# Kernel tuning notes

Measured on AMD Instinct MI355X. Metric: run time of the kernel, lower is better.

## Reference

```python
import jax, jax.numpy as jnp
import numpy as np

H = 16
D = 64  # head_dim = 1024 // 16
SCALE = D ** -0.5


def setup_inputs() -> dict:
    key = jax.random.key(0)
    ks = jax.random.split(key, 12)
    B, N, C = 2, 2048, 1024
    s = C ** -0.5
    return {
        "hidden_states": jax.random.normal(ks[0], (B, N, C), jnp.float32),
        "pos_embeds": jax.random.normal(ks[1], (B, N, C), jnp.float32),
        "Wq": jax.random.normal(ks[2], (C, C), jnp.float32) * s,
        "bq": jnp.zeros((C,), jnp.float32),
        "Wk": jax.random.normal(ks[3], (C, C), jnp.float32) * s,
        "bk": jnp.zeros((C,), jnp.float32),
        "Wv": jax.random.normal(ks[4], (C, C), jnp.float32) * s,
        "bv": jnp.zeros((C,), jnp.float32),
        "Wpos": jax.random.normal(ks[5], (C, C), jnp.float32) * s,
        "pos_bias_u": jax.random.normal(ks[6], (H, D), jnp.float32) * 0.1,
        "pos_bias_v": jax.random.normal(ks[7], (H, D), jnp.float32) * 0.1,
        "Wo": jax.random.normal(ks[8], (C, C), jnp.float32) * s,
        "bo": jnp.zeros((C,), jnp.float32),
    }


def reference(hidden_states, pos_embeds, Wq, bq, Wk, bk, Wv, bv, Wpos,
              pos_bias_u, pos_bias_v, Wo, bo):
    B, N, C = hidden_states.shape
    # projections (torch Linear: y = x @ W.T + b), split heads -> (B, N, H, D)
    q = (hidden_states @ Wq.T + bq).reshape(B, N, H, D)
    k = (hidden_states @ Wk.T + bk).reshape(B, N, H, D)
    v = (hidden_states @ Wv.T + bv).reshape(B, N, H, D)
    p = (pos_embeds @ Wpos.T).reshape(B, N, H, D)
    # relative-position biased logits: matrix_ac + matrix_bd
    q_u = q + pos_bias_u  # (B,N,H,D) + (H,D)
    q_v = q + pos_bias_v
    ac = jnp.einsum('bnhd,bmhd->bhnm', q_u, k)
    bd = jnp.einsum('bnhd,bmhd->bhnm', q_v, p)
    attn = jax.nn.softmax((ac + bd) * SCALE, axis=-1)  # (B,H,N,N)
    out = jnp.einsum('bhnm,bmhd->bnhd', attn, v).reshape(B, N, C)
    return out @ Wo.T + bo
```

## Files before the change

kernel.cpp:

```cpp
#include <hip/hip_runtime.h>
#include <hip/hip_bf16.h>


typedef short bf16x8 __attribute__((ext_vector_type(8)));
typedef float f32x4 __attribute__((ext_vector_type(4)));

#define BB 2
#define NN 2048
#define CC 1024
#define HH 16
#define DD 64
#define MM (BB * NN)
#define SC2E 0.18033688f

__device__ __forceinline__ unsigned short f2bf(float f) {
    union { float f; unsigned int u; } x; x.f = f;
    unsigned int r = x.u + 0x7FFFu + ((x.u >> 16) & 1u);
    return (unsigned short)(r >> 16);
}

__device__ __forceinline__ float bf2f(unsigned short s) {
    union { unsigned int u; float f; } x; x.u = ((unsigned int)s) << 16;
    return x.f;
}

__device__ __forceinline__ unsigned int pk2(float a, float b) {
    __hip_bfloat162 h = __float22bfloat162_rn(make_float2(a, b));
    unsigned int u; __builtin_memcpy(&u, &h, 4); return u;
}

typedef __attribute__((address_space(1))) const unsigned int* gas1_t;
typedef __attribute__((address_space(3))) unsigned int* las3_t;

__device__ __forceinline__ void gload_lds16(const unsigned short* g, unsigned short* l) {
    __builtin_amdgcn_global_load_lds((gas1_t)g, (las3_t)l, 16, 0, 0);
}

__global__ __launch_bounds__(256) void cast_f32_bf16(const float* __restrict__ src,
                                                     unsigned short* __restrict__ dst,
                                                     int n4) {
    int i = blockIdx.x * 256 + threadIdx.x;
    if (i >= n4) return;
    float4 v = ((const float4*)src)[i];
    union { unsigned short s[4]; uint2 u; } p;
    p.s[0] = f2bf(v.x); p.s[1] = f2bf(v.y); p.s[2] = f2bf(v.z); p.s[3] = f2bf(v.w);
    ((uint2*)dst)[i] = p.u;
}

template <int MODE>
__global__ __launch_bounds__(256) void gemm_bt(const unsigned short* __restrict__ A,
                                               const unsigned short* __restrict__ B,
                                               void* __restrict__ out0,
                                               const void* __restrict__ aux,
                                               const float* __restrict__ bias) {
    constexpr int K = CC;
    __shared__ unsigned short As[128 * 32];
    __shared__ unsigned short Bs[64 * 32];
    const int t = threadIdx.x;
    const int w = t >> 6, lane = t & 63, l15 = lane & 15, quad = lane >> 4;
    const int m0 = blockIdx.x * 128, n0 = blockIdx.y * 64;
    const int wm = (w >> 1) * 64, wn = (w & 1) * 32;

    f32x4 acc[4][2];
#pragma unroll
    for (int i = 0; i < 4; ++i)
#pragma unroll
        for (int j = 0; j < 2; ++j)
#pragma unroll
            for (int r = 0; r < 4; ++r) acc[i][j][r] = 0.f;

    for (int kb = 0; kb < K; kb += 32) {
        __syncthreads();
#pragma unroll
        for (int j = 0; j < 2; ++j) {
            int id = j * 256 + t;
            int row = id >> 2, c4 = id & 3;
            gload_lds16(&A[(size_t)(m0 + row) * K + kb + c4 * 8], &As[id * 8]);
        }
        {
            int row = t >> 2, c4 = t & 3;
            gload_lds16(&B[(size_t)(n0 + row) * K + kb + c4 * 8], &Bs[t * 8]);
        }
        __syncthreads();
        bf16x8 af[4], bfr[2];
#pragma unroll
        for (int i = 0; i < 4; ++i)
            af[i] = *(const bf16x8*)&As[(wm + i * 16 + l15) * 32 + quad * 8];
#pragma unroll
        for (int j = 0; j < 2; ++j)
            bfr[j] = *(const bf16x8*)&Bs[(wn + j * 16 + l15) * 32 + quad * 8];
#pragma unroll
        for (int i = 0; i < 4; ++i)
#pragma unroll
            for (int j = 0; j < 2; ++j)
                acc[i][j] = __builtin_amdgcn_mfma_f32_16x16x32_bf16(af[i], bfr[j], acc[i][j], 0, 0, 0);
    }

#pragma unroll
    for (int i = 0; i < 4; ++i) {
#pragma unroll
        for (int j = 0; j < 2; ++j) {
            const int col = n0 + wn + j * 16 + l15;
            const int row_base = m0 + wm + i * 16 + quad * 4;
            const float bc = (MODE == 4) ? 0.f : (bias ? bias[col] : 0.f);
            if (MODE == 0) {
#pragma unroll
                for (int r = 0; r < 4; ++r)
                    ((unsigned short*)out0)[(size_t)(row_base + r) * CC + col] = f2bf(acc[i][j][r] + bc);
            } else if (MODE == 1) {
#pragma unroll
                for (int r = 0; r < 4; ++r)
                    ((unsigned short*)out0)[(size_t)(row_base + r) * CC + col] =
                        f2bf((acc[i][j][r] + bc) * SC2E);
            } else if (MODE == 2) {
#pragma unroll
                for (int r = 0; r < 4; ++r)
                    ((float*)out0)[(size_t)(row_base + r) * CC + col] = acc[i][j][r] + bc;
            } else if (MODE == 4) {
#pragma unroll
                for (int r = 0; r < 4; ++r) {
                    float kv = bf2f(((const unsigned short*)aux)[(size_t)(row_base + r) * CC + col]);
                    ((unsigned short*)out0)[(size_t)(row_base + r) * CC + col] = f2bf(acc[i][j][r] + kv);
                }
            } else {
                const int b = row_base >> 11, nseq = row_base & 2047;
                const int hh = col >> 6, dd = col & 63;
                union { unsigned short s[4]; uint2 u; } pk;
#pragma unroll
                for (int r = 0; r < 4; ++r) pk.s[r] = f2bf(acc[i][j][r] + bc);
                size_t idx = ((size_t)(b * HH + hh) * DD + dd) * NN + nseq;
                *(uint2*)&((unsigned short*)out0)[idx] = pk.u;
            }
        }
    }
}

__global__ __launch_bounds__(256) void fuse_c(const unsigned short* __restrict__ k,
                                              const unsigned short* __restrict__ kp,
                                              const float* __restrict__ pbu,
                                              const float* __restrict__ pbv,
                                              float* __restrict__ c) {
    const int gw = (blockIdx.x * 256 + threadIdx.x) >> 6;
    const int lane = threadIdx.x & 63;
    const int row = gw >> 4, h = gw & 15;
    const size_t off = (size_t)row * CC + h * 64 + lane;
    const float u = pbu[h * 64 + lane], v = pbv[h * 64 + lane];
    float val = (u - v) * bf2f(k[off]) + v * bf2f(kp[off]);
#pragma unroll
    for (int o = 1; o < 64; o <<= 1) val += __shfl_xor(val, o);
    if (lane == 0) {
        const int b = row >> 11, n = row & 2047;
        c[((size_t)(b * HH + h)) * NN + n] = val * SC2E;
    }
}

#define PST 80
__global__ __launch_bounds__(256, 2) void attn_kernel(const unsigned short* __restrict__ q,
                                                      const unsigned short* __restrict__ kp,
                                                      const unsigned short* __restrict__ vt,
                                                      const float* __restrict__ cb,
                                                      unsigned short* __restrict__ att) {
    __shared__ unsigned short Ks[64 * 64];
    __shared__ unsigned short Vs[64 * 64];
    __shared__ unsigned short Ps[4][32 * PST];

    const int t = threadIdx.x;
    const int w = t >> 6, lane = t & 63, l15 = lane & 15, quad = lane >> 4;
    const int qt = blockIdx.x, h = blockIdx.y, b = blockIdx.z;
    const int sw = (l15 & 7) * 8;

    bf16x8 qf[2][2];
#pragma unroll
    for (int qb = 0; qb < 2; ++qb) {
        const int qrow = qt * 128 + w * 32 + qb * 16 + l15;
        const size_t qoff = ((size_t)(b * NN + qrow) * HH + h) * DD;
#pragma unroll
        for (int c2 = 0; c2 < 2; ++c2)
            qf[qb][c2] = *(const bf16x8*)&q[qoff + c2 * 32 + quad * 8];
    }

    f32x4 oT[4][2];
    float l_lane[2] = {0.f, 0.f};
#pragma unroll
    for (int db = 0; db < 4; ++db)
#pragma unroll
        for (int qb = 0; qb < 2; ++qb)
#pragma unroll
            for (int r = 0; r < 4; ++r) oT[db][qb][r] = 0.f;

    const size_t kbase = (size_t)b * NN * CC + (size_t)h * DD;
    const size_t vbase = (size_t)(b * HH + h) * DD * NN;
    const size_t cbase = (size_t)(b * HH + h) * NN;

    for (int kt = 0; kt < NN / 64; ++kt) {
        __syncthreads();
#pragma unroll
        for (int j = 0; j < 2; ++j) {
            int id = j * 256 + t, row = id >> 3, c8 = id & 7;
            int gc = (c8 ^ (row & 7)) * 8;
            gload_lds16(&kp[kbase + (size_t)(kt * 64 + row) * CC + gc], &Ks[id * 8]);
            gload_lds16(&vt[vbase + (size_t)row * NN + kt * 64 + gc], &Vs[id * 8]);
        }
        __syncthreads();

        f32x4 s[2][4];
#pragma unroll
        for (int t4 = 0; t4 < 4; ++t4) {
            f32x4 c4 = *(const f32x4*)&cb[cbase + kt * 64 + t4 * 16 + quad * 4];
            s[0][t4] = c4; s[1][t4] = c4;
        }
#pragma unroll
        for (int t4 = 0; t4 < 4; ++t4) {
            const int row = t4 * 16 + l15;
#pragma unroll
            for (int c2 = 0; c2 < 2; ++c2) {
                bf16x8 kf = *(const bf16x8*)&Ks[row * 64 + ((c2 * 4 + quad) * 8 ^ sw)];
#pragma unroll
                for (int qb = 0; qb < 2; ++qb)
                    s[qb][t4] = __builtin_amdgcn_mfma_f32_16x16x32_bf16(kf, qf[qb][c2], s[qb][t4], 0, 0, 0);
            }
        }

#pragma unroll
        for (int qb = 0; qb < 2; ++qb) {
            float rs = 0.f;
#pragma unroll
            for (int t4 = 0; t4 < 4; ++t4)
#pragma unroll
                for (int r = 0; r < 4; ++r) {
                    float pv = exp2f(s[qb][t4][r]);
                    s[qb][t4][r] = pv;
                    rs += pv;
                }
            l_lane[qb] += rs;
#pragma unroll
            for (int t4 = 0; t4 < 4; ++t4) {
                uint2 pk;
                pk.x = pk2(s[qb][t4][0], s[qb][t4][1]);
                pk.y = pk2(s[qb][t4][2], s[qb][t4][3]);
                *(uint2*)&Ps[w][(qb * 16 + l15) * PST + t4 * 16 + quad * 4] = pk;
            }
        }

#pragma unroll
        for (int c2 = 0; c2 < 2; ++c2) {
            bf16x8 pf[2];
#pragma unroll
            for (int qb = 0; qb < 2; ++qb)
                pf[qb] = *(const bf16x8*)&Ps[w][(qb * 16 + l15) * PST + c2 * 32 + quad * 8];
#pragma unroll
            for (int db = 0; db < 4; ++db) {
                bf16x8 vf = *(const bf16x8*)&Vs[(db * 16 + l15) * 64 + ((c2 * 4 + quad) * 8 ^ sw)];
#pragma unroll
                for (int qb = 0; qb < 2; ++qb)
                    oT[db][qb] = __builtin_amdgcn_mfma_f32_16x16x32_bf16(vf, pf[qb], oT[db][qb], 0, 0, 0);
            }
        }
    }

#pragma unroll
    for (int qb = 0; qb < 2; ++qb) {
        float l = l_lane[qb];
        l += __shfl_xor(l, 16);
        l += __shfl_xor(l, 32);
        const float inv = 1.f / l;
        const int qrow = qt * 128 + w * 32 + qb * 16 + l15;
        const size_t ob = ((size_t)(b * NN + qrow) * HH + h) * DD;
#pragma unroll
        for (int db = 0; db < 4; ++db) {
            uint2 pk;
            pk.x = pk2(oT[db][qb][0] * inv, oT[db][qb][1] * inv);
            pk.y = pk2(oT[db][qb][2] * inv, oT[db][qb][3] * inv);
            *(uint2*)&att[ob + db * 16 + quad * 4] = pk;
        }
    }
}

extern "C" void kernel_launch(void* const* d_in, const int* in_sizes, int n_in,
                              void* d_out, int out_size, void* d_ws, size_t ws_size,
                              hipStream_t stream) {
    const float* hs   = (const float*)d_in[0];
    const float* pos  = (const float*)d_in[1];
    const float* Wq   = (const float*)d_in[2];
    const float* bq   = (const float*)d_in[3];
    const float* Wk   = (const float*)d_in[4];
    const float* bk   = (const float*)d_in[5];
    const float* Wv   = (const float*)d_in[6];
    const float* bv   = (const float*)d_in[7];
    const float* Wpos = (const float*)d_in[8];
    const float* pbu  = (const float*)d_in[9];
    const float* pbv  = (const float*)d_in[10];
    const float* Wo   = (const float*)d_in[11];
    const float* bo   = (const float*)d_in[12];
    float* out = (float*)d_out;

    const size_t nHS = (size_t)MM * CC;
    const size_t nW  = (size_t)CC * CC;

    unsigned short* p = (unsigned short*)d_ws;
    unsigned short* hsb  = p;            p += nHS;
    unsigned short* posb = p;            p += nHS;
    unsigned short* wqb  = p;            p += nW;
    unsigned short* wkb  = p;            p += nW;
    unsigned short* wvb  = p;            p += nW;
    unsigned short* wpb  = p;            p += nW;
    unsigned short* wob  = p;            p += nW;
    unsigned short* qsb  = p;            p += nHS;
    unsigned short* kbf  = p;            p += nHS;
    unsigned short* kpb  = p;            p += nHS;
    unsigned short* vtb  = p;            p += nHS;
    float* cb = (float*)p;               p += (size_t)BB * HH * NN * 2;
    unsigned short* attb = hsb;

    cast_f32_bf16<<<(int)(nHS / 4 / 256), 256, 0, stream>>>(hs, hsb, (int)(nHS / 4));
    cast_f32_bf16<<<(int)(nHS / 4 / 256), 256, 0, stream>>>(pos, posb, (int)(nHS / 4));
    cast_f32_bf16<<<(int)(nW / 4 / 256), 256, 0, stream>>>(Wq, wqb, (int)(nW / 4));
    cast_f32_bf16<<<(int)(nW / 4 / 256), 256, 0, stream>>>(Wk, wkb, (int)(nW / 4));
    cast_f32_bf16<<<(int)(nW / 4 / 256), 256, 0, stream>>>(Wv, wvb, (int)(nW / 4));
    cast_f32_bf16<<<(int)(nW / 4 / 256), 256, 0, stream>>>(Wpos, wpb, (int)(nW / 4));
    cast_f32_bf16<<<(int)(nW / 4 / 256), 256, 0, stream>>>(Wo, wob, (int)(nW / 4));

    dim3 ggrid(MM / 128, CC / 64);
    gemm_bt<1><<<ggrid, 256, 0, stream>>>(hsb, wqb, qsb, nullptr, bq);
    gemm_bt<0><<<ggrid, 256, 0, stream>>>(hsb, wkb, kbf, nullptr, bk);
    gemm_bt<3><<<ggrid, 256, 0, stream>>>(hsb, wvb, vtb, nullptr, bv);
    gemm_bt<4><<<ggrid, 256, 0, stream>>>(posb, wpb, kpb, kbf, nullptr);

    fuse_c<<<MM * HH / 4, 256, 0, stream>>>(kbf, kpb, pbu, pbv, cb);

    dim3 agrid(NN / 128, HH, BB);
    attn_kernel<<<agrid, 256, 0, stream>>>(qsb, kpb, vtb, cb, attb);

    gemm_bt<2><<<ggrid, 256, 0, stream>>>(attb, wob, out, nullptr, bo);
}
```

Before: 301.5 us.

## Fuse casts and QKV GEMMs, concat K|pos, split-K attention with merge

Merges the seven cast launches into one grid. It concatenates hidden and pos inputs so k+p comes out of a single K=2048 GEMM, and batches the Q, KP and V GEMMs into one launch with 128x128 tiles and an LDS-transposed V store. The per-key bias term is now computed algebraically from precomputed weight-bias products instead of from K and P. Attention is split into two key halves for more parallelism, with a merge kernel that normalises the result. The trade-off is extra fp32 partial-output traffic, an extra launch, and different rounding in the bias path.

```diff
diff --git a/kernel.cpp b/kernel.cpp
--- a/kernel.cpp
+++ b/kernel.cpp
@@ -36,23 +36,323 @@
     __builtin_amdgcn_global_load_lds((gas1_t)g, (las3_t)l, 16, 0, 0);
 }
 
-__global__ __launch_bounds__(256) void cast_f32_bf16(const float* __restrict__ src,
-                                                     unsigned short* __restrict__ dst,
-                                                     int n4) {
-    int i = blockIdx.x * 256 + threadIdx.x;
-    if (i >= n4) return;
-    float4 v = ((const float4*)src)[i];
-    union { unsigned short s[4]; uint2 u; } p;
-    p.s[0] = f2bf(v.x); p.s[1] = f2bf(v.y); p.s[2] = f2bf(v.z); p.s[3] = f2bf(v.w);
-    ((uint2*)dst)[i] = p.u;
-}
-
-template <int MODE>
-__global__ __launch_bounds__(256) void gemm_bt(const unsigned short* __restrict__ A,
-                                               const unsigned short* __restrict__ B,
-                                               void* __restrict__ out0,
-                                               const void* __restrict__ aux,
-                                               const float* __restrict__ bias) {
+struct CastArgs {
+    const float* src[7];
+    unsigned short* dst[7];
+    int rows[7];
+    int stride[7];
+    int col0[7];
+};
+__global__ __launch_bounds__(256) void cast_all(CastArgs a) {
+    const int seg = blockIdx.y, row = blockIdx.x;
+    if (row >= a.rows[seg]) return;
+    const int c4 = threadIdx.x;
+    float4 v = ((const float4*)a.src[seg])[row * 256 + c4];
+    uint2 u;
+    u.x = pk2(v.x, v.y);
+    u.y = pk2(v.z, v.w);
+    ((uint2*)(a.dst[seg] + (size_t)row * a.stride[seg] + a.col0[seg]))[c4] = u;
+}
+
+__global__ __launch_bounds__(256) void prep(const float* __restrict__ Wk,
+                                            const float* __restrict__ Wp,
+                                            const float* __restrict__ pbu,
+                                            const float* __restrict__ pbv,
+                                            const float* __restrict__ bk,
+                                            float* __restrict__ Wc,
+                                            float* __restrict__ cu) {
+    const int h = blockIdx.x, half = blockIdx.y;
+    const float* W = half ? Wp : Wk;
+    const float* uv = half ? pbv : pbu;
+    const int c0 = threadIdx.x * 4;
+    float a0 = 0.f, a1 = 0.f, a2 = 0.f, a3 = 0.f;
+    for (int d = 0; d < 64; ++d) {
+        const float wgt = uv[h * 64 + d] * SC2E;
+        float4 wv = *(const float4*)&W[(size_t)(h * 64 + d) * 1024 + c0];
+        a0 += wgt * wv.x; a1 += wgt * wv.y; a2 += wgt * wv.z; a3 += wgt * wv.w;
+    }
+    float4 o = make_float4(a0, a1, a2, a3);
+    *(float4*)&Wc[(size_t)h * 2048 + half * 1024 + c0] = o;
+    if (half == 0 && threadIdx.x < 64) {
+        const int d = threadIdx.x;
+        float v = pbu[h * 64 + d] * bk[h * 64 + d] * SC2E;
+#pragma unroll
+        for (int o2 = 1; o2 < 64; o2 <<= 1) v += __shfl_xor(v, o2);
+        if (d == 0) cu[h] = v;
+    }
+}
+
+struct QkpvArgs {
+    const unsigned short* A;
+    const unsigned short* B[3];
+    unsigned short* out[3];
+    const float* bias[3];
+    int K[3];
+};
+__global__ __launch_bounds__(256) void gemm_qkpv(QkpvArgs g) {
+    __shared__ unsigned short As[128 * 32];
+    __shared__ unsigned short Bs[128 * 32];
+    __shared__ unsigned short Tr[4][64 * 72];
+    const int z = blockIdx.z;
+    const int K = g.K[z];
+    const unsigned short* __restrict__ A = g.A;
+    const unsigned short* __restrict__ B = g.B[z];
+    const float* __restrict__ bias = g.bias[z];
+    const int t = threadIdx.x;
+    const int w = t >> 6, lane = t & 63, l15 = lane & 15, quad = lane >> 4;
+    const int m0 = blockIdx.x * 128, n0 = blockIdx.y * 128;
+    const int wm = (w >> 1) * 64, wn = (w & 1) * 64;
+
+    f32x4 acc[4][4];
+#pragma unroll
+    for (int i = 0; i < 4; ++i)
+#pragma unroll
+        for (int j = 0; j < 4; ++j)
+#pragma unroll
+            for (int r = 0; r < 4; ++r) acc[i][j][r] = 0.f;
+
+    for (int kb = 0; kb < K; kb += 32) {
+        __syncthreads();
+#pragma unroll
+        for (int j = 0; j < 2; ++j) {
+            int id = j * 256 + t;
+            int row = id >> 2, c4 = (id & 3) * 8;
+            gload_lds16(&A[(size_t)(m0 + row) * 2048 + kb + c4], &As[id * 8]);
+            gload_lds16(&B[(size_t)(n0 + row) * K + kb + c4], &Bs[id * 8]);
+        }
+        __syncthreads();
+        bf16x8 af[4], bfr[4];
+#pragma unroll
+        for (int i = 0; i < 4; ++i)
+            af[i] = *(const bf16x8*)&As[(wm + i * 16 + l15) * 32 + quad * 8];
+#pragma unroll
+        for (int j = 0; j < 4; ++j)
+            bfr[j] = *(const bf16x8*)&Bs[(wn + j * 16 + l15) * 32 + quad * 8];
+#pragma unroll
+        for (int i = 0; i < 4; ++i)
+#pragma unroll
+            for (int j = 0; j < 4; ++j)
+                acc[i][j] = __builtin_amdgcn_mfma_f32_16x16x32_bf16(af[i], bfr[j], acc[i][j], 0, 0, 0);
+    }
+
+    if (z != 2) {
+        const float sc = (z == 0) ? SC2E : 1.f;
+        unsigned short* __restrict__ out = g.out[z];
+#pragma unroll
+        for (int i = 0; i < 4; ++i)
+#pragma unroll
+            for (int j = 0; j < 4; ++j) {
+                const int col = n0 + wn + j * 16 + l15;
+                const int row_base = m0 + wm + i * 16 + quad * 4;
+                const float bc = bias[col];
+#pragma unroll
+                for (int r = 0; r < 4; ++r)
+                    out[(size_t)(row_base + r) * CC + col] = f2bf((acc[i][j][r] + bc) * sc);
+            }
+    } else {
+        unsigned short* __restrict__ out = g.out[2];
+#pragma unroll
+        for (int i = 0; i < 4; ++i)
+#pragma unroll
+            for (int j = 0; j < 4; ++j) {
+                const int col = n0 + wn + j * 16 + l15;
+                const float bc = bias[col];
+                union { unsigned short s[4]; uint2 u; } pk;
+#pragma unroll
+                for (int r = 0; r < 4; ++r) pk.s[r] = f2bf(acc[i][j][r] + bc);
+                *(uint2*)&Tr[w][(j * 16 + l15) * 72 + i * 16 + quad * 4] = pk.u;
+            }
+        const int bI = (m0 + wm) >> 11, nseq0 = (m0 + wm) & 2047;
+        const int rl = lane >> 3, cl = (lane & 7) * 8;
+#pragma unroll
+        for (int pass = 0; pass < 8; ++pass) {
+            const int ln = pass * 8 + rl;
+            uint4 vv = *(const uint4*)&Tr[w][ln * 72 + cl];
+            const int col = n0 + wn + ln;
+            const int hh = col >> 6, dd = col & 63;
+            *(uint4*)&out[((size_t)(bI * 16 + hh) * 64 + dd) * 2048 + nseq0 + cl] = vv;
+        }
+    }
+}
+
+__global__ __launch_bounds__(256) void gemm_c(const unsigned short* __restrict__ hp,
+                                              const float* __restrict__ Wc,
+                                              const float* __restrict__ cu,
+                                              float* __restrict__ cb) {
+    const int gw = (blockIdx.x * 256 + threadIdx.x) >> 6;
+    const int lane = threadIdx.x & 63;
+    const unsigned short* rowp = hp + (size_t)gw * 2048;
+    float a[32];
+#pragma unroll
+    for (int c = 0; c < 4; ++c) {
+        bf16x8 v = *(const bf16x8*)&rowp[c * 512 + lane * 8];
+#pragma unroll
+        for (int j = 0; j < 8; ++j) a[c * 8 + j] = bf2f((unsigned short)v[j]);
+    }
+    float mine = 0.f;
+    for (int h = 0; h < HH; ++h) {
+        float acc = 0.f;
+#pragma unroll
+        for (int c = 0; c < 4; ++c) {
+            const float* wp = &Wc[(size_t)h * 2048 + c * 512 + lane * 8];
+            float4 w0 = *(const float4*)wp;
+            float4 w1 = *(const float4*)(wp + 4);
+            acc += a[c*8+0]*w0.x + a[c*8+1]*w0.y + a[c*8+2]*w0.z + a[c*8+3]*w0.w
+                 + a[c*8+4]*w1.x + a[c*8+5]*w1.y + a[c*8+6]*w1.z + a[c*8+7]*w1.w;
+        }
+#pragma unroll
+        for (int o = 1; o < 64; o <<= 1) acc += __shfl_xor(acc, o);
+        if (lane == h) mine = acc + cu[h];
+    }
+    if (lane < HH) {
+        const int b = gw >> 11, n = gw & 2047;
+        cb[((size_t)(b * HH + lane)) * NN + n] = mine;
+    }
+}
+
+#define PST 80
+__global__ __launch_bounds__(256) void attn_kernel(const unsigned short* __restrict__ q,
+                                                   const unsigned short* __restrict__ kp,
+                                                   const unsigned short* __restrict__ vt,
+                                                   const float* __restrict__ cb,
+                                                   float* __restrict__ opart,
+                                                   float* __restrict__ lpart) {
+    __shared__ unsigned short Ks[64 * 64];
+    __shared__ unsigned short Vs[64 * 64];
+    __shared__ unsigned short Ps[4][32 * PST];
+
+    const int t = threadIdx.x;
+    const int w = t >> 6, lane = t & 63, l15 = lane & 15, quad = lane >> 4;
+    const int qt = blockIdx.x, h = blockIdx.y, z = blockIdx.z;
+    const int b = z >> 1, kz = z & 1;
+    const int sw = (l15 & 7) * 8;
+
+    bf16x8 qf[2][2];
+#pragma unroll
+    for (int qb = 0; qb < 2; ++qb) {
+        const int qrow = qt * 128 + w * 32 + qb * 16 + l15;
+        const size_t qoff = ((size_t)(b * NN + qrow) * HH + h) * DD;
+#pragma unroll
+        for (int c2 = 0; c2 < 2; ++c2)
+            qf[qb][c2] = *(const bf16x8*)&q[qoff + c2 * 32 + quad * 8];
+    }
+
+    f32x4 oT[4][2];
+    float l_lane[2] = {0.f, 0.f};
+#pragma unroll
+    for (int db = 0; db < 4; ++db)
+#pragma unroll
+        for (int qb = 0; qb < 2; ++qb)
+#pragma unroll
+            for (int r = 0; r < 4; ++r) oT[db][qb][r] = 0.f;
+
+    const size_t kbase = (size_t)b * NN * CC + (size_t)h * DD;
+    const size_t vbase = (size_t)(b * HH + h) * DD * NN;
+    const size_t cbase = (size_t)(b * HH + h) * NN;
+
+    for (int kt = kz * 16; kt < kz * 16 + 16; ++kt) {
+        __syncthreads();
+#pragma unroll
+        for (int j = 0; j < 2; ++j) {
+            int id = j * 256 + t, row = id >> 3, c8 = id & 7;
+            int gc = (c8 ^ (row & 7)) * 8;
+            gload_lds16(&kp[kbase + (size_t)(kt * 64 + row) * CC + gc], &Ks[id * 8]);
+            gload_lds16(&vt[vbase + (size_t)row * NN + kt * 64 + gc], &Vs[id * 8]);
+        }
+        __syncthreads();
+
+        f32x4 s[2][4];
+#pragma unroll
+        for (int t4 = 0; t4 < 4; ++t4) {
+            f32x4 c4 = *(const f32x4*)&cb[cbase + kt * 64 + t4 * 16 + quad * 4];
+            s[0][t4] = c4; s[1][t4] = c4;
+        }
+#pragma unroll
+        for (int t4 = 0; t4 < 4; ++t4) {
+            const int row = t4 * 16 + l15;
+#pragma unroll
+            for (int c2 = 0; c2 < 2; ++c2) {
+                bf16x8 kf = *(const bf16x8*)&Ks[row * 64 + ((c2 * 4 + quad) * 8 ^ sw)];
+#pragma unroll
+                for (int qb = 0; qb < 2; ++qb)
+                    s[qb][t4] = __builtin_amdgcn_mfma_f32_16x16x32_bf16(kf, qf[qb][c2], s[qb][t4], 0, 0, 0);
+            }
+        }
+
+#pragma unroll
+        for (int qb = 0; qb < 2; ++qb) {
+            float rs = 0.f;
+#pragma unroll
+            for (int t4 = 0; t4 < 4; ++t4)
+#pragma unroll
+                for (int r = 0; r < 4; ++r) {
+                    float pv = exp2f(s[qb][t4][r]);
+                    s[qb][t4][r] = pv;
+                    rs += pv;
+                }
+            l_lane[qb] += rs;
+#pragma unroll
+            for (int t4 = 0; t4 < 4; ++t4) {
+                uint2 pk;
+                pk.x = pk2(s[qb][t4][0], s[qb][t4][1]);
+                pk.y = pk2(s[qb][t4][2], s[qb][t4][3]);
+                *(uint2*)&Ps[w][(qb * 16 + l15) * PST + t4 * 16 + quad * 4] = pk;
+            }
+        }
+
+#pragma unroll
+        for (int c2 = 0; c2 < 2; ++c2) {
+            bf16x8 pf[2];
+#pragma unroll
+            for (int qb = 0; qb < 2; ++qb)
+                pf[qb] = *(const bf16x8*)&Ps[w][(qb * 16 + l15) * PST + c2 * 32 + quad * 8];
+#pragma unroll
+            for (int db = 0; db < 4; ++db) {
+                bf16x8 vf = *(const bf16x8*)&Vs[(db * 16 + l15) * 64 + ((c2 * 4 + quad) * 8 ^ sw)];
+#pragma unroll
+                for (int qb = 0; qb < 2; ++qb)
+                    oT[db][qb] = __builtin_amdgcn_mfma_f32_16x16x32_bf16(vf, pf[qb], oT[db][qb], 0, 0, 0);
+            }
+        }
+    }
+
+#pragma unroll
+    for (int qb = 0; qb < 2; ++qb) {
+        float l = l_lane[qb];
+        l += __shfl_xor(l, 16);
+        l += __shfl_xor(l, 32);
+        const int qrow = qt * 128 + w * 32 + qb * 16 + l15;
+        const size_t ob = (((size_t)(kz * 2 + b) * HH + h) * NN + qrow) * DD;
+#pragma unroll
+        for (int db = 0; db < 4; ++db)
+            *(f32x4*)&opart[ob + db * 16 + quad * 4] = oT[db][qb];
+        if (quad == 0)
+            lpart[((size_t)(kz * 2 + b) * HH + h) * NN + qrow] = l;
+    }
+}
+
+__global__ __launch_bounds__(256) void merge_kernel(const float* __restrict__ opart,
+                                                    const float* __restrict__ lpart,
+                                                    unsigned short* __restrict__ att) {
+    const int idx = blockIdx.x * 256 + threadIdx.x;
+    const int d4 = idx & 15, qn = (idx >> 4) & 2047, h = (idx >> 15) & 15, b = idx >> 19;
+    const size_t i0 = (((size_t)b * HH + h) * NN + qn) * DD + d4 * 4;
+    const size_t i1 = (((size_t)(2 + b) * HH + h) * NN + qn) * DD + d4 * 4;
+    f32x4 o0 = *(const f32x4*)&opart[i0];
+    f32x4 o1 = *(const f32x4*)&opart[i1];
+    const float l = lpart[((size_t)b * HH + h) * NN + qn] +
+                    lpart[((size_t)(2 + b) * HH + h) * NN + qn];
+    const float inv = 1.f / l;
+    uint2 pk;
+    pk.x = pk2((o0[0] + o1[0]) * inv, (o0[1] + o1[1]) * inv);
+    pk.y = pk2((o0[2] + o1[2]) * inv, (o0[3] + o1[3]) * inv);
+    *(uint2*)&att[(((size_t)b * NN + qn) * HH + h) * DD + d4 * 4] = pk;
+}
+
+__global__ __launch_bounds__(256) void gemm_out(const unsigned short* __restrict__ A,
+                                                const unsigned short* __restrict__ B,
+                                                float* __restrict__ out,
+                                                const float* __restrict__ bias) {
     constexpr int K = CC;
     __shared__ unsigned short As[128 * 32];
     __shared__ unsigned short Bs[64 * 32];
@@ -74,12 +374,12 @@
 #pragma unroll
         for (int j = 0; j < 2; ++j) {
             int id = j * 256 + t;
-            int row = id >> 2, c4 = id & 3;
-            gload_lds16(&A[(size_t)(m0 + row) * K + kb + c4 * 8], &As[id * 8]);
+            int row = id >> 2, c4 = (id & 3) * 8;
+            gload_lds16(&A[(size_t)(m0 + row) * K + kb + c4], &As[id * 8]);
         }
         {
-            int row = t >> 2, c4 = t & 3;
-            gload_lds16(&B[(size_t)(n0 + row) * K + kb + c4 * 8], &Bs[t * 8]);
+            int row = t >> 2, c4 = (t & 3) * 8;
+            gload_lds16(&B[(size_t)(n0 + row) * K + kb + c4], &Bs[t * 8]);
         }
         __syncthreads();
         bf16x8 af[4], bfr[2];
@@ -97,183 +397,16 @@
     }
 
 #pragma unroll
-    for (int i = 0; i < 4; ++i) {
+    for (int i = 0; i < 4; ++i)
 #pragma unroll
         for (int j = 0; j < 2; ++j) {
             const int col = n0 + wn + j * 16 + l15;
             const int row_base = m0 + wm + i * 16 + quad * 4;
-            const float bc = (MODE == 4) ? 0.f : (bias ? bias[col] : 0.f);
-            if (MODE == 0) {
-#pragma unroll
-                for (int r = 0; r < 4; ++r)
-                    ((unsigned short*)out0)[(size_t)(row_base + r) * CC + col] = f2bf(acc[i][j][r] + bc);
-            } else if (MODE == 1) {
-#pragma unroll
-                for (int r = 0; r < 4; ++r)
-                    ((unsigned short*)out0)[(size_t)(row_base + r) * CC + col] =
-                        f2bf((acc[i][j][r] + bc) * SC2E);
-            } else if (MODE == 2) {
-#pragma unroll
-                for (int r = 0; r < 4; ++r)
-                    ((float*)out0)[(size_t)(row_base + r) * CC + col] = acc[i][j][r] + bc;
-            } else if (MODE == 4) {
-#pragma unroll
-                for (int r = 0; r < 4; ++r) {
-                    float kv = bf2f(((const unsigned short*)aux)[(size_t)(row_base + r) * CC + col]);
-                    ((unsigned short*)out0)[(size_t)(row_base + r) * CC + col] = f2bf(acc[i][j][r] + kv);
-                }
-            } else {
-                const int b = row_base >> 11, nseq = row_base & 2047;
-                const int hh = col >> 6, dd = col & 63;
-                union { unsigned short s[4]; uint2 u; } pk;
-#pragma unroll
-                for (int r = 0; r < 4; ++r) pk.s[r] = f2bf(acc[i][j][r] + bc);
-                size_t idx = ((size_t)(b * HH + hh) * DD + dd) * NN + nseq;
-                *(uint2*)&((unsigned short*)out0)[idx] = pk.u;
-            }
-        }
-    }
-}
-
-__global__ __launch_bounds__(256) void fuse_c(const unsigned short* __restrict__ k,
-                                              const unsigned short* __restrict__ kp,
-                                              const float* __restrict__ pbu,
-                                              const float* __restrict__ pbv,
-                                              float* __restrict__ c) {
-    const int gw = (blockIdx.x * 256 + threadIdx.x) >> 6;
-    const int lane = threadIdx.x & 63;
-    const int row = gw >> 4, h = gw & 15;
-    const size_t off = (size_t)row * CC + h * 64 + lane;
-    const float u = pbu[h * 64 + lane], v = pbv[h * 64 + lane];
-    float val = (u - v) * bf2f(k[off]) + v * bf2f(kp[off]);
-#pragma unroll
-    for (int o = 1; o < 64; o <<= 1) val += __shfl_xor(val, o);
-    if (lane == 0) {
-        const int b = row >> 11, n = row & 2047;
-        c[((size_t)(b * HH + h)) * NN + n] = val * SC2E;
-    }
-}
-
-#define PST 80
-__global__ __launch_bounds__(256, 2) void attn_kernel(const unsigned short* __restrict__ q,
-                                                      const unsigned short* __restrict__ kp,
-                                                      const unsigned short* __restrict__ vt,
-                                                      const float* __restrict__ cb,
-                                                      unsigned short* __restrict__ att) {
-    __shared__ unsigned short Ks[64 * 64];
-    __shared__ unsigned short Vs[64 * 64];
-    __shared__ unsigned short Ps[4][32 * PST];
-
-    const int t = threadIdx.x;
-    const int w = t >> 6, lane = t & 63, l15 = lane & 15, quad = lane >> 4;
-    const int qt = blockIdx.x, h = blockIdx.y, b = blockIdx.z;
-    const int sw = (l15 & 7) * 8;
-
-    bf16x8 qf[2][2];
-#pragma unroll
-    for (int qb = 0; qb < 2; ++qb) {
-        const int qrow = qt * 128 + w * 32 + qb * 16 + l15;
-        const size_t qoff = ((size_t)(b * NN + qrow) * HH + h) * DD;
-#pragma unroll
-        for (int c2 = 0; c2 < 2; ++c2)
-            qf[qb][c2] = *(const bf16x8*)&q[qoff + c2 * 32 + quad * 8];
-    }
-
-    f32x4 oT[4][2];
-    float l_lane[2] = {0.f, 0.f};
-#pragma unroll
-    for (int db = 0; db < 4; ++db)
-#pragma unroll
-        for (int qb = 0; qb < 2; ++qb)
-#pragma unroll
-            for (int r = 0; r < 4; ++r) oT[db][qb][r] = 0.f;
-
-    const size_t kbase = (size_t)b * NN * CC + (size_t)h * DD;
-    const size_t vbase = (size_t)(b * HH + h) * DD * NN;
-    const size_t cbase = (size_t)(b * HH + h) * NN;
-
-    for (int kt = 0; kt < NN / 64; ++kt) {
-        __syncthreads();
-#pragma unroll
-        for (int j = 0; j < 2; ++j) {
-            int id = j * 256 + t, row = id >> 3, c8 = id & 7;
-            int gc = (c8 ^ (row & 7)) * 8;
-            gload_lds16(&kp[kbase + (size_t)(kt * 64 + row) * CC + gc], &Ks[id * 8]);
-            gload_lds16(&vt[vbase + (size_t)row * NN + kt * 64 + gc], &Vs[id * 8]);
-        }
-        __syncthreads();
-
-        f32x4 s[2][4];
-#pragma unroll
-        for (int t4 = 0; t4 < 4; ++t4) {
-            f32x4 c4 = *(const f32x4*)&cb[cbase + kt * 64 + t4 * 16 + quad * 4];
-            s[0][t4] = c4; s[1][t4] = c4;
-        }
-#pragma unroll
-        for (int t4 = 0; t4 < 4; ++t4) {
-            const int row = t4 * 16 + l15;
-#pragma unroll
-            for (int c2 = 0; c2 < 2; ++c2) {
-                bf16x8 kf = *(const bf16x8*)&Ks[row * 64 + ((c2 * 4 + quad) * 8 ^ sw)];
-#pragma unroll
-                for (int qb = 0; qb < 2; ++qb)
-                    s[qb][t4] = __builtin_amdgcn_mfma_f32_16x16x32_bf16(kf, qf[qb][c2], s[qb][t4], 0, 0, 0);
-            }
-        }
-
-#pragma unroll
-        for (int qb = 0; qb < 2; ++qb) {
-            float rs = 0.f;
-#pragma unroll
-            for (int t4 = 0; t4 < 4; ++t4)
-#pragma unroll
-                for (int r = 0; r < 4; ++r) {
-                    float pv = exp2f(s[qb][t4][r]);
-                    s[qb][t4][r] = pv;
-                    rs += pv;
-                }
-            l_lane[qb] += rs;
-#pragma unroll
-            for (int t4 = 0; t4 < 4; ++t4) {
-                uint2 pk;
-                pk.x = pk2(s[qb][t4][0], s[qb][t4][1]);
-                pk.y = pk2(s[qb][t4][2], s[qb][t4][3]);
-                *(uint2*)&Ps[w][(qb * 16 + l15) * PST + t4 * 16 + quad * 4] = pk;
-            }
-        }
-
-#pragma unroll
-        for (int c2 = 0; c2 < 2; ++c2) {
-            bf16x8 pf[2];
-#pragma unroll
-            for (int qb = 0; qb < 2; ++qb)
-                pf[qb] = *(const bf16x8*)&Ps[w][(qb * 16 + l15) * PST + c2 * 32 + quad * 8];
-#pragma unroll
-            for (int db = 0; db < 4; ++db) {
-                bf16x8 vf = *(const bf16x8*)&Vs[(db * 16 + l15) * 64 + ((c2 * 4 + quad) * 8 ^ sw)];
-#pragma unroll
-                for (int qb = 0; qb < 2; ++qb)
-                    oT[db][qb] = __builtin_amdgcn_mfma_f32_16x16x32_bf16(vf, pf[qb], oT[db][qb], 0, 0, 0);
-            }
-        }
-    }
-
-#pragma unroll
-    for (int qb = 0; qb < 2; ++qb) {
-        float l = l_lane[qb];
-        l += __shfl_xor(l, 16);
-        l += __shfl_xor(l, 32);
-        const float inv = 1.f / l;
-        const int qrow = qt * 128 + w * 32 + qb * 16 + l15;
-        const size_t ob = ((size_t)(b * NN + qrow) * HH + h) * DD;
-#pragma unroll
-        for (int db = 0; db < 4; ++db) {
-            uint2 pk;
-            pk.x = pk2(oT[db][qb][0] * inv, oT[db][qb][1] * inv);
-            pk.y = pk2(oT[db][qb][2] * inv, oT[db][qb][3] * inv);
-            *(uint2*)&att[ob + db * 16 + quad * 4] = pk;
-        }
-    }
+            const float bc = bias[col];
+#pragma unroll
+            for (int r = 0; r < 4; ++r)
+                out[(size_t)(row_base + r) * CC + col] = acc[i][j][r] + bc;
+        }
 }
 
 extern "C" void kernel_launch(void* const* d_in, const int* in_sizes, int n_in,
@@ -294,42 +427,51 @@
     const float* bo   = (const float*)d_in[12];
     float* out = (float*)d_out;
 
-    const size_t nHS = (size_t)MM * CC;
-    const size_t nW  = (size_t)CC * CC;
-
-    unsigned short* p = (unsigned short*)d_ws;
-    unsigned short* hsb  = p;            p += nHS;
-    unsigned short* posb = p;            p += nHS;
-    unsigned short* wqb  = p;            p += nW;
-    unsigned short* wkb  = p;            p += nW;
-    unsigned short* wvb  = p;            p += nW;
-    unsigned short* wpb  = p;            p += nW;
-    unsigned short* wob  = p;            p += nW;
-    unsigned short* qsb  = p;            p += nHS;
-    unsigned short* kbf  = p;            p += nHS;
-    unsigned short* kpb  = p;            p += nHS;
-    unsigned short* vtb  = p;            p += nHS;
-    float* cb = (float*)p;               p += (size_t)BB * HH * NN * 2;
-    unsigned short* attb = hsb;
-
-    cast_f32_bf16<<<(int)(nHS / 4 / 256), 256, 0, stream>>>(hs, hsb, (int)(nHS / 4));
-    cast_f32_bf16<<<(int)(nHS / 4 / 256), 256, 0, stream>>>(pos, posb, (int)(nHS / 4));
-    cast_f32_bf16<<<(int)(nW / 4 / 256), 256, 0, stream>>>(Wq, wqb, (int)(nW / 4));
-    cast_f32_bf16<<<(int)(nW / 4 / 256), 256, 0, stream>>>(Wk, wkb, (int)(nW / 4));
-    cast_f32_bf16<<<(int)(nW / 4 / 256), 256, 0, stream>>>(Wv, wvb, (int)(nW / 4));
-    cast_f32_bf16<<<(int)(nW / 4 / 256), 256, 0, stream>>>(Wpos, wpb, (int)(nW / 4));
-    cast_f32_bf16<<<(int)(nW / 4 / 256), 256, 0, stream>>>(Wo, wob, (int)(nW / 4));
-
-    dim3 ggrid(MM / 128, CC / 64);
-    gemm_bt<1><<<ggrid, 256, 0, stream>>>(hsb, wqb, qsb, nullptr, bq);
-    gemm_bt<0><<<ggrid, 256, 0, stream>>>(hsb, wkb, kbf, nullptr, bk);
-    gemm_bt<3><<<ggrid, 256, 0, stream>>>(hsb, wvb, vtb, nullptr, bv);
-    gemm_bt<4><<<ggrid, 256, 0, stream>>>(posb, wpb, kpb, kbf, nullptr);
-
-    fuse_c<<<MM * HH / 4, 256, 0, stream>>>(kbf, kpb, pbu, pbv, cb);
-
-    dim3 agrid(NN / 128, HH, BB);
-    attn_kernel<<<agrid, 256, 0, stream>>>(qsb, kpb, vtb, cb, attb);
-
-    gemm_bt<2><<<ggrid, 256, 0, stream>>>(attb, wob, out, nullptr, bo);
-}
+    char* base = (char*)d_ws;
+    unsigned short* hp    = (unsigned short*)(base);
+    unsigned short* wqb   = (unsigned short*)(base + 16777216);
+    unsigned short* wkpb  = (unsigned short*)(base + 18874368);
+    unsigned short* wvb   = (unsigned short*)(base + 23068672);
+    float*          opart = (float*)(base);
+    unsigned short* wob   = (unsigned short*)(base + 33554432);
+    float*          Wc    = (float*)(base + 35651584);
+    float*          cu    = (float*)(base + 35782656);
+    float*          cb    = (float*)(base + 35783168);
+    unsigned short* qsb   = (unsigned short*)(base + 36045312);
+    unsigned short* kpb   = (unsigned short*)(base + 44433920);
+    unsigned short* vtb   = (unsigned short*)(base + 52822528);
+    float*          lpart = (float*)(base + 61211136);
+    unsigned short* attb  = qsb;
+
+    CastArgs ca;
+    ca.src[0] = hs;   ca.dst[0] = hp;   ca.rows[0] = 4096; ca.stride[0] = 2048; ca.col0[0] = 0;
+    ca.src[1] = pos;  ca.dst[1] = hp;   ca.rows[1] = 4096; ca.stride[1] = 2048; ca.col0[1] = 1024;
+    ca.src[2] = Wq;   ca.dst[2] = wqb;  ca.rows[2] = 1024; ca.stride[2] = 1024; ca.col0[2] = 0;
+    ca.src[3] = Wk;   ca.dst[3] = wkpb; ca.rows[3] = 1024; ca.stride[3] = 2048; ca.col0[3] = 0;
+    ca.src[4] = Wpos; ca.dst[4] = wkpb; ca.rows[4] = 1024; ca.stride[4] = 2048; ca.col0[4] = 1024;
+    ca.src[5] = Wv;   ca.dst[5] = wvb;  ca.rows[5] = 1024; ca.stride[5] = 1024; ca.col0[5] = 0;
+    ca.src[6] = Wo;   ca.dst[6] = wob;  ca.rows[6] = 1024; ca.stride[6] = 1024; ca.col0[6] = 0;
+    dim3 cgrid(4096, 7);
+    cast_all<<<cgrid, 256, 0, stream>>>(ca);
+
+    dim3 pgrid(HH, 2);
+    prep<<<pgrid, 256, 0, stream>>>(Wk, Wpos, pbu, pbv, bk, Wc, cu);
+
+    QkpvArgs qa;
+    qa.A = hp;
+    qa.B[0] = wqb;  qa.out[0] = qsb; qa.bias[0] = bq; qa.K[0] = 1024;
+    qa.B[1] = wkpb; qa.out[1] = kpb; qa.bias[1] = bk; qa.K[1] = 2048;
+    qa.B[2] = wvb;  qa.out[2] = vtb; qa.bias[2] = bv; qa.K[2] = 1024;
+    dim3 ggrid(MM / 128, CC / 128, 3);
+    gemm_qkpv<<<ggrid, 256, 0, stream>>>(qa);
+
+    gemm_c<<<MM / 4, 256, 0, stream>>>(hp, Wc, cu, cb);
+
+    dim3 agrid(NN / 128, HH, 4);
+    attn_kernel<<<agrid, 256, 0, stream>>>(qsb, kpb, vtb, cb, opart, lpart);
+
+    merge_kernel<<<(BB * NN * HH * DD / 4) / 256, 256, 0, stream>>>(opart, lpart, attb);
+
+    dim3 ogrid(MM / 128, CC / 64);
+    gemm_out<<<ogrid, 256, 0, stream>>>(attb, wob, out, bo);
+}
```

Measured after the change: 304.8 us. No clear change (+1.1%).
